# Optimization experiments

Measured on AMD Instinct MI355X. Metric: run time of the kernel, lower is better.

The kernel has to match this reference:

```python
import jax, jax.numpy as jnp
import numpy as np
from jax import lax

VOCAB = 32000
H = 1024
T = 4096


def setup_inputs() -> dict:
    key = jax.random.key(0)
    ks = jax.random.split(key, 6)
    s = 1.0 / np.sqrt(H)  # PyTorch GRU init scale
    x = jax.random.randint(ks[0], (T,), 0, VOCAB)
    embedding = jax.random.normal(ks[1], (VOCAB, H), dtype=jnp.float32)
    # direction 0 = 'forward', direction 1 = 'reverse' (both run left-to-right
    # here because the original feeds one timestep at a time)
    w_ih = jax.random.uniform(ks[2], (2, 3 * H, H), jnp.float32, -s, s)
    w_hh = jax.random.uniform(ks[3], (2, 3 * H, H), jnp.float32, -s, s)
    b_ih = jax.random.uniform(ks[4], (2, 3 * H), jnp.float32, -s, s)
    b_hh = jax.random.uniform(ks[5], (2, 3 * H), jnp.float32, -s, s)
    return {"x": x, "embedding": embedding, "w_ih": w_ih, "w_hh": w_hh,
            "b_ih": b_ih, "b_hh": b_hh}


def reference(x, embedding, w_ih, w_hh, b_ih, b_hh):
    emb = embedding[x]  # (T, H)
    # Precompute input-side gate projections for both directions: (T, 2, 3H)
    x_proj = jnp.einsum('th,dgh->tdg', emb, w_ih) + b_ih

    def step(h, xp):  # h: (2, H), xp: (2, 3H)
        hp = jnp.einsum('dh,dgh->dg', h, w_hh) + b_hh  # (2, 3H)
        xr, xz, xn = xp[:, :H], xp[:, H:2 * H], xp[:, 2 * H:]
        hr, hz, hn = hp[:, :H], hp[:, H:2 * H], hp[:, 2 * H:]
        r = jax.nn.sigmoid(xr + hr)
        z = jax.nn.sigmoid(xz + hz)
        n = jnp.tanh(xn + r * hn)
        h_new = (1.0 - z) * n + z * h
        return h_new, h_new

    h0 = jnp.zeros((2, H), emb.dtype)
    h_last, hs = lax.scan(step, h0, x_proj)  # hs: (T, 2, H)
    # per-step output = concat(dir0_hidden, dir1_hidden) -> (T, 2H)
    outputs = hs.reshape(T, 2 * H)
    # final hidden = sum of the two direction hiddens, shape (1, H)
    hidden = (h_last[0] + h_last[1])[None, :]
    return outputs, hidden
```

## Files before the change

kernel.cpp:

```cpp
#include <hip/hip_runtime.h>
#include <hip/hip_bf16.h>
#include <stdint.h>

#define HDIM 1024
#define TSEQ 4096
#define GATES3 3072
#define NTOT 6144

#define COMM_OFF (64u * 1024 * 1024)
#define XFIN_OFF (COMM_OFF + 32768)

typedef __attribute__((ext_vector_type(8))) short short8;
typedef __attribute__((ext_vector_type(4))) float f32x4;
typedef __attribute__((ext_vector_type(4))) unsigned int ux4;

__device__ __forceinline__ unsigned short f2bf(float f) {
    uint32_t u = __float_as_uint(f);
    uint32_t r = (u + 0x7FFFu + ((u >> 16) & 1u)) >> 16;
    return (unsigned short)r;
}
__device__ __forceinline__ float bf2f(unsigned short s) {
    return __uint_as_float(((uint32_t)s) << 16);
}

__device__ __forceinline__ ux4 ld16_sys(const void* p) {
    ux4 r;
    asm volatile("global_load_dwordx4 %0, %1, off sc0 sc1\n\ts_waitcnt vmcnt(0)"
                 : "=v"(r) : "v"(p) : "memory");
    return r;
}

__global__ __launch_bounds__(256) void init_comm_kernel(uint8_t* __restrict__ wsb) {
    int i = blockIdx.x * 256 + threadIdx.x;
    unsigned long long* comm = (unsigned long long*)(wsb + COMM_OFF);
    unsigned long long* xfin = (unsigned long long*)(wsb + XFIN_OFF);
    if (i < 4096) comm[i] = ~0ull;
    if (i < 1024) xfin[i] = ~0ull;
}

__global__ __launch_bounds__(256) void xproj_gemm_kernel(
    const int* __restrict__ x, const float* __restrict__ emb,
    const float* __restrict__ w_ih, const float* __restrict__ b_ih,
    unsigned short* __restrict__ rz, float* __restrict__ n32)
{
    __shared__ short As[128][32];
    __shared__ short Bs[128][32];

    const int tid = threadIdx.x;
    const int m0 = blockIdx.x * 128;
    const int n0 = blockIdx.y * 128;

    const int srow = tid >> 1;
    const int half = tid & 1;

    const int arow_g = x[m0 + srow];
    const float* aptr = emb + (size_t)arow_g * HDIM + half * 16;
    const float* bptr = w_ih + (size_t)(n0 + srow) * HDIM + half * 16;

    const int wid = tid >> 6;
    const int lane = tid & 63;
    const int wm = wid >> 1;
    const int wn = wid & 1;
    const int l15 = lane & 15;
    const int ksel = (lane >> 4) * 8;

    f32x4 acc[4][4];
    f32x4 zero4 = {0.f, 0.f, 0.f, 0.f};
#pragma unroll
    for (int mi = 0; mi < 4; mi++)
#pragma unroll
        for (int ni = 0; ni < 4; ni++) acc[mi][ni] = zero4;

    for (int k0 = 0; k0 < HDIM; k0 += 32) {
        float4 av[4], bv[4];
#pragma unroll
        for (int jj = 0; jj < 4; jj++) {
            av[jj] = *(const float4*)(aptr + k0 + jj * 4);
            bv[jj] = *(const float4*)(bptr + k0 + jj * 4);
        }
        if (k0) __syncthreads();
        short ta[16], tb[16];
#pragma unroll
        for (int jj = 0; jj < 4; jj++) {
            ta[jj*4+0] = f2bf(av[jj].x); ta[jj*4+1] = f2bf(av[jj].y);
            ta[jj*4+2] = f2bf(av[jj].z); ta[jj*4+3] = f2bf(av[jj].w);
            tb[jj*4+0] = f2bf(bv[jj].x); tb[jj*4+1] = f2bf(bv[jj].y);
            tb[jj*4+2] = f2bf(bv[jj].z); tb[jj*4+3] = f2bf(bv[jj].w);
        }
        *(short8*)&As[srow][half * 16]     = *(short8*)&ta[0];
        *(short8*)&As[srow][half * 16 + 8] = *(short8*)&ta[8];
        *(short8*)&Bs[srow][half * 16]     = *(short8*)&tb[0];
        *(short8*)&Bs[srow][half * 16 + 8] = *(short8*)&tb[8];
        __syncthreads();

        short8 af[4], bfr[4];
#pragma unroll
        for (int mi = 0; mi < 4; mi++)
            af[mi] = *(const short8*)&As[wm * 64 + mi * 16 + l15][ksel];
#pragma unroll
        for (int ni = 0; ni < 4; ni++)
            bfr[ni] = *(const short8*)&Bs[wn * 64 + ni * 16 + l15][ksel];
#pragma unroll
        for (int mi = 0; mi < 4; mi++)
#pragma unroll
            for (int ni = 0; ni < 4; ni++)
                acc[mi][ni] = __builtin_amdgcn_mfma_f32_16x16x32_bf16(
                    af[mi], bfr[ni], acc[mi][ni], 0, 0, 0);
    }

    const int r0 = m0 + wm * 64;
    const int c0 = n0 + wn * 64;
#pragma unroll
    for (int mi = 0; mi < 4; mi++) {
#pragma unroll
        for (int ni = 0; ni < 4; ni++) {
            int c = c0 + ni * 16 + l15;
            int dir = (c >= GATES3) ? 1 : 0;
            int g3 = c - dir * GATES3;
            int gate = g3 >> 10;
            int jj = g3 & 1023;
            float bias = b_ih[c];
#pragma unroll
            for (int v = 0; v < 4; v++) {
                int r = r0 + mi * 16 + (lane >> 4) * 4 + v;
                float val = acc[mi][ni][v] + bias;
                if (gate < 2)
                    rz[(size_t)r * 4096 + dir * 2048 + gate * 1024 + jj] = f2bf(val);
                else
                    n32[(size_t)r * 2048 + dir * 1024 + jj] = val;
            }
        }
    }
}

__global__ __launch_bounds__(512, 1) void rnn_kernel(
    const unsigned short* __restrict__ rz, const float* __restrict__ n32,
    const float* __restrict__ w_hh, const float* __restrict__ b_hh,
    uint8_t* __restrict__ wsb, float* __restrict__ out)
{
    __shared__ float h_lds[2][1088];

    uint8_t* comm = wsb + COMM_OFF;
    unsigned long long* xfin = (unsigned long long*)(wsb + XFIN_OFF);

    const int tid = threadIdx.x;
    const int bid = blockIdx.x;
    const int dir = bid >> 5;
    const int role = bid & 31;
    const int g   = tid >> 4;
    const int sl  = tid & 15;
    const int j   = role * 32 + g;

    f32x4 w0[16], w1[16], w2[16];
    {
        const float* Wd = w_hh + (size_t)dir * GATES3 * HDIM;
        const float* p0 = Wd + ((size_t)(0 * HDIM + j)) * HDIM + sl * 64;
        const float* p1 = Wd + ((size_t)(1 * HDIM + j)) * HDIM + sl * 64;
        const float* p2 = Wd + ((size_t)(2 * HDIM + j)) * HDIM + sl * 64;
#pragma unroll
        for (int c4 = 0; c4 < 16; c4++) {
            w0[c4] = *(const f32x4*)(p0 + c4 * 4);
            w1[c4] = *(const f32x4*)(p1 + c4 * 4);
            w2[c4] = *(const f32x4*)(p2 + c4 * 4);
        }
    }
    float bh0 = 0.f, bh1 = 0.f, bh2 = 0.f;
    if (sl == 0) {
        bh0 = b_hh[dir * GATES3 + j];
        bh1 = b_hh[dir * GATES3 + HDIM + j];
        bh2 = b_hh[dir * GATES3 + 2 * HDIM + j];
    }

    uint8_t* commD = comm + dir * 8192;
    const uint8_t* poll0 = commD + (size_t)tid * 16;
    const uint8_t* poll1 = poll0 + 16384;
    unsigned long long* slot0 = (unsigned long long*)(commD) + j;
    unsigned long long* slot1 = (unsigned long long*)(commD + 16384) + j;

    const int idx0 = 2 * tid + 4 * (tid >> 5);
    const unsigned short* rzp = rz + dir * 2048 + j;
    const float* np = n32 + dir * 1024 + j;
    const int ocol = role * 32 + 2 * tid;
    const int oidx = ocol + 4 * (ocol >> 6);

    float last_h = 0.f;

    for (int t = 0; t < TSEQ; t++) {
        const int buf = t & 1;

        float xr = 0.f, xz = 0.f, xn = 0.f;
        if (sl == 0) {
            xr = bf2f(rzp[0]);
            xz = bf2f(rzp[1024]);
            xn = np[0];
        }
        rzp += 4096; np += 2048;

        if (t == 0) {
            h_lds[0][idx0]     = 0.f;
            h_lds[0][idx0 + 1] = 0.f;
        } else {
            const uint32_t want = (uint32_t)(t - 1);
            const uint8_t* src = ((t - 1) & 1) ? poll1 : poll0;
            ux4 v;
            do { v = ld16_sys(src); } while (v.x != want || v.z != want);
            h_lds[buf][idx0]     = __uint_as_float(v.y);
            h_lds[buf][idx0 + 1] = __uint_as_float(v.w);
        }
        __syncthreads();

        if (t > 0 && tid < 16) {
            float2 hv = *(float2*)&h_lds[buf][oidx];
            *(float2*)(out + (size_t)(t - 1) * 2048 + dir * 1024 + ocol) = hv;
        }

        f32x4 s0 = {0,0,0,0}, s1 = {0,0,0,0}, s2 = {0,0,0,0};
        const float* hb = &h_lds[buf][sl * 68];
#pragma unroll
        for (int c4 = 0; c4 < 16; c4++) {
            f32x4 hv = *(const f32x4*)(hb + c4 * 4);
            s0 += w0[c4] * hv;
            s1 += w1[c4] * hv;
            s2 += w2[c4] * hv;
        }
        float a0 = s0.x + s0.y + s0.z + s0.w;
        float a1 = s1.x + s1.y + s1.z + s1.w;
        float a2 = s2.x + s2.y + s2.z + s2.w;
#pragma unroll
        for (int m = 1; m < 16; m <<= 1) {
            a0 += __shfl_xor(a0, m, 16);
            a1 += __shfl_xor(a1, m, 16);
            a2 += __shfl_xor(a2, m, 16);
        }

        if (sl == 0) {
            float r  = 1.f / (1.f + __expf(-(xr + a0 + bh0)));
            float z  = 1.f / (1.f + __expf(-(xz + a1 + bh1)));
            float y  = xn + r * (a2 + bh2);
            float e2 = __expf(2.f * y);
            float n_ = 1.f - 2.f / (e2 + 1.f);
            float hp = h_lds[buf][j + 4 * (j >> 6)];
            float hnew = z * (hp - n_) + n_;
            last_h = hnew;
            unsigned long long pack =
                ((unsigned long long)__float_as_uint(hnew) << 32) | (uint32_t)t;
            __hip_atomic_store((t & 1) ? slot1 : slot0, pack,
                               __ATOMIC_RELAXED, __HIP_MEMORY_SCOPE_AGENT);
        }
    }

    if (sl == 0)
        out[(size_t)(TSEQ - 1) * 2048 + dir * 1024 + j] = last_h;

    if (dir == 1 && sl == 0) {
        unsigned long long pack =
            ((unsigned long long)__float_as_uint(last_h) << 32) | 0x0BADF00Du;
        __hip_atomic_store(&xfin[j], pack, __ATOMIC_RELAXED, __HIP_MEMORY_SCOPE_AGENT);
    }
    if (dir == 0 && sl == 0) {
        unsigned long long v;
        do {
            v = __hip_atomic_load(&xfin[j], __ATOMIC_RELAXED, __HIP_MEMORY_SCOPE_AGENT);
        } while ((uint32_t)v != 0x0BADF00Du);
        out[(size_t)TSEQ * 2048 + j] = last_h + __uint_as_float((uint32_t)(v >> 32));
    }
}

extern "C" void kernel_launch(void* const* d_in, const int* in_sizes, int n_in,
                              void* d_out, int out_size, void* d_ws, size_t ws_size,
                              hipStream_t stream)
{
    const int*   x     = (const int*)d_in[0];
    const float* emb   = (const float*)d_in[1];
    const float* w_ih  = (const float*)d_in[2];
    const float* w_hh  = (const float*)d_in[3];
    const float* b_ih  = (const float*)d_in[4];
    const float* b_hh  = (const float*)d_in[5];
    float* out = (float*)d_out;

    unsigned short* rz  = (unsigned short*)d_ws;
    float* n32 = (float*)((char*)d_ws + (size_t)TSEQ * 4096 * 2);
    uint8_t* wsb = (uint8_t*)d_ws;

    init_comm_kernel<<<16, 256, 0, stream>>>(wsb);

    dim3 g(TSEQ / 128, NTOT / 128);
    xproj_gemm_kernel<<<g, 256, 0, stream>>>(x, emb, w_ih, b_ih, rz, n32);

    const unsigned short* a0 = rz;
    const float* a1 = n32;
    const float* a2 = w_hh;
    const float* a3 = b_hh;
    uint8_t* a4 = wsb;
    float* a5 = out;
    void* args[] = { (void*)&a0, (void*)&a1, (void*)&a2, (void*)&a3, (void*)&a4, (void*)&a5 };
    hipLaunchCooperativeKernel((void*)rnn_kernel, dim3(64), dim3(512), args, 0, stream);
}
```

Measured before the change: 7.797 ms.

## Co-locate each direction's workgroups on one XCD and poll with cheaper cache scope

The launch grows to 256 workgroups, and only those with blockIdx%8 in {0,1} do work. This assumes round-robin XCD placement, so each direction's 32 workgroups land on one XCD and can exchange hidden state through the shared L2 (sc0 loads and stores) instead of the system-coherent path. A token handshake checks at runtime that the workgroups really see each other's sc0 writes. If the check fails they fall back to the old coherent path, and a slow-path mirror buffer with periodic sc0|sc1 polling guards against stalls. The goal is lower per-step communication latency in the serial recurrence. The cost is extra idle workgroups, dependence on undocumented placement, and a more complex protocol.

```diff
diff --git a/kernel.cpp b/kernel.cpp
--- a/kernel.cpp
+++ b/kernel.cpp
@@ -7,12 +7,17 @@
 #define GATES3 3072
 #define NTOT 6144
 
-#define COMM_OFF (64u * 1024 * 1024)
-#define XFIN_OFF (COMM_OFF + 32768)
+#define COMM_OFF  (64u * 1024 * 1024)
+#define XFIN_OFF  (COMM_OFF + 32768)
+#define TOK_OFF   (COMM_OFF + 40960)
+#define OK_OFF    (COMM_OFF + 49152)
+#define COMM2_OFF (COMM_OFF + 65536)
 
 typedef __attribute__((ext_vector_type(8))) short short8;
 typedef __attribute__((ext_vector_type(4))) float f32x4;
 typedef __attribute__((ext_vector_type(4))) unsigned int ux4;
+typedef __attribute__((ext_vector_type(2))) unsigned int ux2;
+typedef unsigned long long u64;
 
 __device__ __forceinline__ unsigned short f2bf(float f) {
     uint32_t u = __float_as_uint(f);
@@ -23,19 +28,44 @@
     return __uint_as_float(((uint32_t)s) << 16);
 }
 
+template<int FAST>
+__device__ __forceinline__ ux4 poll16(const void* p) {
+    ux4 r;
+    if constexpr (FAST)
+        asm volatile("global_load_dwordx4 %0, %1, off sc0\n\ts_waitcnt vmcnt(0)"
+                     : "=v"(r) : "v"(p) : "memory");
+    else
+        asm volatile("global_load_dwordx4 %0, %1, off sc1\n\ts_waitcnt vmcnt(0)"
+                     : "=v"(r) : "v"(p) : "memory");
+    return r;
+}
 __device__ __forceinline__ ux4 ld16_sys(const void* p) {
     ux4 r;
     asm volatile("global_load_dwordx4 %0, %1, off sc0 sc1\n\ts_waitcnt vmcnt(0)"
                  : "=v"(r) : "v"(p) : "memory");
     return r;
 }
+__device__ __forceinline__ void st8_sc0(void* p, ux2 v) {
+    asm volatile("global_store_dwordx2 %0, %1, off sc0" :: "v"(p), "v"(v) : "memory");
+}
+__device__ __forceinline__ ux2 ld8_sc0(const void* p) {
+    ux2 r;
+    asm volatile("global_load_dwordx2 %0, %1, off sc0\n\ts_waitcnt vmcnt(0)"
+                 : "=v"(r) : "v"(p) : "memory");
+    return r;
+}
 
 __global__ __launch_bounds__(256) void init_comm_kernel(uint8_t* __restrict__ wsb) {
     int i = blockIdx.x * 256 + threadIdx.x;
-    unsigned long long* comm = (unsigned long long*)(wsb + COMM_OFF);
-    unsigned long long* xfin = (unsigned long long*)(wsb + XFIN_OFF);
-    if (i < 4096) comm[i] = ~0ull;
+    u64* comm  = (u64*)(wsb + COMM_OFF);
+    u64* comm2 = (u64*)(wsb + COMM2_OFF);
+    u64* xfin  = (u64*)(wsb + XFIN_OFF);
+    u64* tok   = (u64*)(wsb + TOK_OFF);
+    uint32_t* ok = (uint32_t*)(wsb + OK_OFF);
+    if (i < 4096) { comm[i] = ~0ull; comm2[i] = ~0ull; }
     if (i < 1024) xfin[i] = ~0ull;
+    if (i < 512)  tok[i] = 0ull;
+    if (i < 64)   ok[i] = 0u;
 }
 
 __global__ __launch_bounds__(256) void xproj_gemm_kernel(
@@ -133,20 +163,18 @@
     }
 }
 
-__global__ __launch_bounds__(512, 1) void rnn_kernel(
-    const unsigned short* __restrict__ rz, const float* __restrict__ n32,
-    const float* __restrict__ w_hh, const float* __restrict__ b_hh,
-    uint8_t* __restrict__ wsb, float* __restrict__ out)
+template<int FAST>
+__device__ void run_gru(float (*h_lds)[1088], int dir, int role,
+                        const unsigned short* __restrict__ rz,
+                        const float* __restrict__ n32,
+                        const float* __restrict__ w_hh,
+                        const float* __restrict__ b_hh,
+                        uint8_t* wsb, float* __restrict__ out)
 {
-    __shared__ float h_lds[2][1088];
-
     uint8_t* comm = wsb + COMM_OFF;
-    unsigned long long* xfin = (unsigned long long*)(wsb + XFIN_OFF);
+    u64* xfin = (u64*)(wsb + XFIN_OFF);
 
     const int tid = threadIdx.x;
-    const int bid = blockIdx.x;
-    const int dir = bid >> 5;
-    const int role = bid & 31;
     const int g   = tid >> 4;
     const int sl  = tid & 15;
     const int j   = role * 32 + g;
@@ -174,10 +202,11 @@
     uint8_t* commD = comm + dir * 8192;
     const uint8_t* poll0 = commD + (size_t)tid * 16;
     const uint8_t* poll1 = poll0 + 16384;
-    unsigned long long* slot0 = (unsigned long long*)(commD) + j;
-    unsigned long long* slot1 = (unsigned long long*)(commD + 16384) + j;
+    uint8_t* slot0 = commD + (size_t)j * 8;
+    uint8_t* slot1 = slot0 + 16384;
 
     const int idx0 = 2 * tid + 4 * (tid >> 5);
+    const int jidx = j + 4 * (j >> 6);
     const unsigned short* rzp = rz + dir * 2048 + j;
     const float* np = n32 + dir * 1024 + j;
     const int ocol = role * 32 + 2 * tid;
@@ -203,7 +232,18 @@
             const uint32_t want = (uint32_t)(t - 1);
             const uint8_t* src = ((t - 1) & 1) ? poll1 : poll0;
             ux4 v;
-            do { v = ld16_sys(src); } while (v.x != want || v.z != want);
+            int spins = 0;
+            for (;;) {
+                v = poll16<FAST>(src);
+                if (v.x == want && v.z == want) break;
+                if (++spins > (1 << 16)) {
+                    v = ld16_sys(src + (COMM2_OFF - COMM_OFF));
+                    if (v.x == want && v.z == want) break;
+                    v = ld16_sys(src);
+                    if (v.x == want && v.z == want) break;
+                    spins = (1 << 15);
+                }
+            }
             h_lds[buf][idx0]     = __uint_as_float(v.y);
             h_lds[buf][idx0 + 1] = __uint_as_float(v.w);
         }
@@ -239,13 +279,21 @@
             float y  = xn + r * (a2 + bh2);
             float e2 = __expf(2.f * y);
             float n_ = 1.f - 2.f / (e2 + 1.f);
-            float hp = h_lds[buf][j + 4 * (j >> 6)];
+            float hp = h_lds[buf][jidx];
             float hnew = z * (hp - n_) + n_;
             last_h = hnew;
-            unsigned long long pack =
-                ((unsigned long long)__float_as_uint(hnew) << 32) | (uint32_t)t;
-            __hip_atomic_store((t & 1) ? slot1 : slot0, pack,
-                               __ATOMIC_RELAXED, __HIP_MEMORY_SCOPE_AGENT);
+            uint8_t* sp = (t & 1) ? slot1 : slot0;
+            ux2 pk; pk.x = (uint32_t)t; pk.y = __float_as_uint(hnew);
+            if constexpr (FAST) {
+                st8_sc0(sp, pk);
+                u64 pack = ((u64)pk.y << 32) | pk.x;
+                __hip_atomic_store((u64*)(sp + (COMM2_OFF - COMM_OFF)), pack,
+                                   __ATOMIC_RELAXED, __HIP_MEMORY_SCOPE_AGENT);
+            } else {
+                u64 pack = ((u64)pk.y << 32) | pk.x;
+                __hip_atomic_store((u64*)sp, pack,
+                                   __ATOMIC_RELAXED, __HIP_MEMORY_SCOPE_AGENT);
+            }
         }
     }
 
@@ -253,17 +301,80 @@
         out[(size_t)(TSEQ - 1) * 2048 + dir * 1024 + j] = last_h;
 
     if (dir == 1 && sl == 0) {
-        unsigned long long pack =
-            ((unsigned long long)__float_as_uint(last_h) << 32) | 0x0BADF00Du;
+        u64 pack = ((u64)__float_as_uint(last_h) << 32) | 0x0BADF00Du;
         __hip_atomic_store(&xfin[j], pack, __ATOMIC_RELAXED, __HIP_MEMORY_SCOPE_AGENT);
     }
     if (dir == 0 && sl == 0) {
-        unsigned long long v;
+        u64 v;
         do {
             v = __hip_atomic_load(&xfin[j], __ATOMIC_RELAXED, __HIP_MEMORY_SCOPE_AGENT);
         } while ((uint32_t)v != 0x0BADF00Du);
         out[(size_t)TSEQ * 2048 + j] = last_h + __uint_as_float((uint32_t)(v >> 32));
     }
+}
+
+__global__ __launch_bounds__(512, 1) void rnn_kernel(
+    const unsigned short* __restrict__ rz, const float* __restrict__ n32,
+    const float* __restrict__ w_hh, const float* __restrict__ b_hh,
+    uint8_t* __restrict__ wsb, float* __restrict__ out)
+{
+    __shared__ float h_lds[2][1088];
+
+    const int tid = threadIdx.x;
+    const int bid = blockIdx.x;
+    const int octet = bid & 7;
+    if (octet >= 2) return;
+    const int dir = octet;
+    const int role = bid >> 3;
+
+    uint8_t* tokD = wsb + TOK_OFF + dir * 2048;
+    uint32_t* okD = (uint32_t*)(wsb + OK_OFF) + dir * 32;
+
+    const uint32_t M1a = 0xA11C0DE5u, M1b = 0xD00DFEEDu;
+    const uint32_t M2a = 0x5EC09D20u, M2b = 0xD2FACE01u;
+    if (tid == 0) { ux2 m; m.x = M1a; m.y = M1b; st8_sc0(tokD + role * 64, m); }
+    int good1 = 0;
+    {
+        int mine = (tid >= 32) ? 1 : 0;
+        const uint8_t* tp = tokD + (tid & 31) * 64;
+        for (int round = 0; round < 300 && !good1; round++) {
+            if (!mine) {
+                ux2 v = ld8_sc0(tp);
+                if (v.x == M1a && v.y == M1b) mine = 1;
+            }
+            good1 = __syncthreads_and(mine);
+        }
+    }
+    if (tid == 0) { ux2 m; m.x = M2a; m.y = M2b; st8_sc0(tokD + role * 64, m); }
+    int good2 = 0;
+    {
+        int mine = (tid >= 32) ? 1 : 0;
+        const uint8_t* tp = tokD + (tid & 31) * 64;
+        for (int round = 0; round < 80 && !good2; round++) {
+            if (!mine) {
+                ux2 v = ld8_sc0(tp);
+                if (v.x == M2a && v.y == M2b) mine = 1;
+            }
+            good2 = __syncthreads_and(mine);
+        }
+    }
+    if (tid == 0)
+        __hip_atomic_store(&okD[role], (good1 && good2) ? 1u : 2u,
+                           __ATOMIC_RELAXED, __HIP_MEMORY_SCOPE_AGENT);
+    int myfast = 1;
+    if (tid < 32) {
+        uint32_t v;
+        do {
+            v = __hip_atomic_load(&okD[tid], __ATOMIC_RELAXED, __HIP_MEMORY_SCOPE_AGENT);
+        } while (v == 0u);
+        myfast = (v == 1u) ? 1 : 0;
+    }
+    const int allfast = __syncthreads_and(myfast);
+
+    if (allfast)
+        run_gru<1>(h_lds, dir, role, rz, n32, w_hh, b_hh, wsb, out);
+    else
+        run_gru<0>(h_lds, dir, role, rz, n32, w_hh, b_hh, wsb, out);
 }
 
 extern "C" void kernel_launch(void* const* d_in, const int* in_sizes, int n_in,
@@ -282,7 +393,7 @@
     float* n32 = (float*)((char*)d_ws + (size_t)TSEQ * 4096 * 2);
     uint8_t* wsb = (uint8_t*)d_ws;
 
-    init_comm_kernel<<<16, 256, 0, stream>>>(wsb);
+    init_comm_kernel<<<32, 256, 0, stream>>>(wsb);
 
     dim3 g(TSEQ / 128, NTOT / 128);
     xproj_gemm_kernel<<<g, 256, 0, stream>>>(x, emb, w_ih, b_ih, rz, n32);
@@ -294,5 +405,5 @@
     uint8_t* a4 = wsb;
     float* a5 = out;
     void* args[] = { (void*)&a0, (void*)&a1, (void*)&a2, (void*)&a3, (void*)&a4, (void*)&a5 };
-    hipLaunchCooperativeKernel((void*)rnn_kernel, dim3(64), dim3(512), args, 0, stream);
-}
+    hipLaunchCooperativeKernel((void*)rnn_kernel, dim3(256), dim3(512), args, 0, stream);
+}
```

Measured after the change: 8.310 ms. +6.6%, slower.
